# Performance work log

Measured on AMD Instinct MI355X. Metric: run time of the kernel, lower is better.

The kernel has to match this reference:

```python
import jax, jax.numpy as jnp
import numpy as np

IGNORE_INDEX = -100


def setup_inputs() -> dict:
    key = jax.random.key(0)
    k1, k2, k3 = jax.random.split(key, 3)
    N, H, V = 8192, 4096, 32000
    x = jax.random.normal(k1, (N, H), dtype=jnp.float32)
    # kaiming_uniform-like init scale for weight (V, H)
    bound = float(np.sqrt(6.0 / H))
    weight = jax.random.uniform(k2, (V, H), dtype=jnp.float32, minval=-bound, maxval=bound)
    target = jax.random.randint(k3, (N,), 0, V, dtype=jnp.int64)
    return {"x": x, "weight": weight, "target": target}


def reference(x, weight, target):
    # Fused linear (lm_head) + cross entropy, reduction='mean', ignore_index=-100.
    # logits: (N, V)
    logits = jnp.einsum('nh,vh->nv', x, weight)
    logp = jax.nn.log_softmax(logits, axis=-1)
    valid = target != IGNORE_INDEX
    safe_tgt = jnp.where(valid, target, 0)
    # NLL of the target class per token
    nll = -jnp.take_along_axis(logp, safe_tgt[:, None], axis=1)[:, 0]
    nll = jnp.where(valid, nll, 0.0)
    denom = jnp.maximum(valid.sum(), 1).astype(nll.dtype)
    return nll.sum() / denom
```

## Files before the change

### kernel.cpp

```cpp
#include <hip/hip_runtime.h>
#include <hip/hip_bf16.h>
#include <stdint.h>

typedef __attribute__((ext_vector_type(8))) __bf16 bf16x8;
typedef __attribute__((ext_vector_type(8))) unsigned short us8;
typedef __attribute__((ext_vector_type(4))) float f32x4;

#define BM 128
#define BN 128
#define BK 64

__device__ inline float bf2f(unsigned short u) {
  unsigned v = ((unsigned)u) << 16;
  float f;
  __builtin_memcpy(&f, &v, 4);
  return f;
}

__device__ inline unsigned short f2bf(float f) {
  unsigned u;
  __builtin_memcpy(&u, &f, 4);
  unsigned r = 0x7FFFu + ((u >> 16) & 1u);
  u += r;
  return (unsigned short)(u >> 16);
}

__device__ inline void gload16(const void* g, void* l) {
  __builtin_amdgcn_global_load_lds(
      (const __attribute__((address_space(1))) unsigned int*)g,
      (__attribute__((address_space(3))) unsigned int*)l, 16, 0, 0);
}

__global__ void cvt_kernel(const float* __restrict__ in,
                           unsigned short* __restrict__ out, int n4) {
  int i = blockIdx.x * blockDim.x + threadIdx.x;
  int stride = gridDim.x * blockDim.x;
  const float4* in4 = reinterpret_cast<const float4*>(in);
  ushort4* out4 = reinterpret_cast<ushort4*>(out);
  for (int idx = i; idx < n4; idx += stride) {
    float4 v = in4[idx];
    ushort4 o;
    o.x = f2bf(v.x); o.y = f2bf(v.y); o.z = f2bf(v.z); o.w = f2bf(v.w);
    out4[idx] = o;
  }
}

__launch_bounds__(256, 2)
__global__ void gemm_lse_kernel(const unsigned short* __restrict__ xb,
                                const unsigned short* __restrict__ wb,
                                float* __restrict__ pm, float* __restrict__ ps,
                                int N, int H, int V) {
  __shared__ __align__(16) unsigned short Als[BM * BK];
  __shared__ __align__(16) unsigned short Bls[BN * BK];

  const int tid = threadIdx.x;
  const int l = tid & 63;
  const int w = tid >> 6;
  const int wr = w >> 1, wc = w & 1;

  const int nwg = gridDim.x;
  const int chunk = nwg >> 3;
  const int id = blockIdx.x;
  const int sid = (id & 7) * chunk + (id >> 3);
  const int num_mb = N / BM;
  const int mb = sid % num_mb;
  const int vb = sid / num_mb;

  const int brow = mb * BM;
  const int bcol = vb * BN;

  f32x4 acc[4][4];
#pragma unroll
  for (int mi = 0; mi < 4; ++mi)
#pragma unroll
    for (int ni = 0; ni < 4; ++ni)
      acc[mi][ni] = (f32x4){0.f, 0.f, 0.f, 0.f};

  const int lrow = l >> 3;
  const int lcol = (l & 7) * 8;

  for (int kt = 0; kt < H; kt += BK) {
#pragma unroll
    for (int t = 0; t < 4; ++t) {
      const int c = w * 4 + t;
      const unsigned short* src =
          xb + (size_t)(brow + c * 8 + lrow) * H + kt + lcol;
      gload16(src, &Als[c * 512]);
    }
#pragma unroll
    for (int t = 0; t < 4; ++t) {
      const int c = w * 4 + t;
      const unsigned short* src =
          wb + (size_t)(bcol + c * 8 + lrow) * H + kt + lcol;
      gload16(src, &Bls[c * 512]);
    }
    __syncthreads();

#pragma unroll
    for (int ks = 0; ks < 2; ++ks) {
      bf16x8 af[4], bfr[4];
#pragma unroll
      for (int mi = 0; mi < 4; ++mi)
        af[mi] = *reinterpret_cast<const bf16x8*>(
            &Als[(wr * 64 + mi * 16 + (l & 15)) * BK + ks * 32 + (l >> 4) * 8]);
#pragma unroll
      for (int ni = 0; ni < 4; ++ni)
        bfr[ni] = *reinterpret_cast<const bf16x8*>(
            &Bls[(wc * 64 + ni * 16 + (l & 15)) * BK + ks * 32 + (l >> 4) * 8]);
#pragma unroll
      for (int mi = 0; mi < 4; ++mi)
#pragma unroll
        for (int ni = 0; ni < 4; ++ni)
          acc[mi][ni] = __builtin_amdgcn_mfma_f32_16x16x32_bf16(
              af[mi], bfr[ni], acc[mi][ni], 0, 0, 0);
    }
    __syncthreads();
  }

  float mrow[4][4], srow[4][4];
#pragma unroll
  for (int mi = 0; mi < 4; ++mi) {
#pragma unroll
    for (int j = 0; j < 4; ++j) {
      float m = acc[mi][0][j];
#pragma unroll
      for (int ni = 1; ni < 4; ++ni) m = fmaxf(m, acc[mi][ni][j]);
#pragma unroll
      for (int off = 1; off < 16; off <<= 1)
        m = fmaxf(m, __shfl_xor(m, off, 64));
      float s = 0.f;
#pragma unroll
      for (int ni = 0; ni < 4; ++ni) s += __expf(acc[mi][ni][j] - m);
#pragma unroll
      for (int off = 1; off < 16; off <<= 1) s += __shfl_xor(s, off, 64);
      mrow[mi][j] = m;
      srow[mi][j] = s;
    }
  }

  float* red_m = (float*)(void*)Als;
  float* red_s = red_m + 256;
  if ((l & 15) == 0) {
    const int g = l >> 4;
#pragma unroll
    for (int mi = 0; mi < 4; ++mi)
#pragma unroll
      for (int j = 0; j < 4; ++j) {
        const int row = wr * 64 + mi * 16 + g * 4 + j;
        red_m[wc * 128 + row] = mrow[mi][j];
        red_s[wc * 128 + row] = srow[mi][j];
      }
  }
  __syncthreads();
  if (tid < 128) {
    const int row = tid;
    const float m0 = red_m[row], m1 = red_m[128 + row];
    const float s0 = red_s[row], s1 = red_s[128 + row];
    const float M = fmaxf(m0, m1);
    const float S = s0 * __expf(m0 - M) + s1 * __expf(m1 - M);
    const size_t o = (size_t)vb * N + brow + row;
    pm[o] = M;
    ps[o] = S;
  }
}

__global__ void reduce_kernel(const float* __restrict__ pm,
                              const float* __restrict__ ps,
                              const unsigned short* __restrict__ xb,
                              const unsigned short* __restrict__ wb,
                              const int* __restrict__ tgt,
                              float* __restrict__ accum,
                              int N, int H, int nvb) {
  const int l = threadIdx.x & 63;
  const int w = threadIdx.x >> 6;
  const int row = blockIdx.x * 4 + w;
  if (row >= N) return;

  float M = -INFINITY, S = 0.f;
  for (int vb = l; vb < nvb; vb += 64) {
    const float m = pm[(size_t)vb * N + row];
    const float s = ps[(size_t)vb * N + row];
    const float nM = fmaxf(M, m);
    S = S * __expf(M - nM) + s * __expf(m - nM);
    M = nM;
  }
#pragma unroll
  for (int off = 1; off < 64; off <<= 1) {
    const float om = __shfl_xor(M, off, 64);
    const float os = __shfl_xor(S, off, 64);
    const float nM = fmaxf(M, om);
    S = S * __expf(M - nM) + os * __expf(om - nM);
    M = nM;
  }

  const int t = tgt[row];
  const bool valid = (t != -100);
  float dot = 0.f;
  if (valid) {
    const unsigned short* xr = xb + (size_t)row * H;
    const unsigned short* wrow = wb + (size_t)t * H;
    for (int k = l * 8; k < H; k += 64 * 8) {
      const us8 xv = *reinterpret_cast<const us8*>(xr + k);
      const us8 wv = *reinterpret_cast<const us8*>(wrow + k);
#pragma unroll
      for (int j = 0; j < 8; ++j) dot += bf2f(xv[j]) * bf2f(wv[j]);
    }
#pragma unroll
    for (int off = 1; off < 64; off <<= 1) dot += __shfl_xor(dot, off, 64);
  }

  if (l == 0) {
    const float lse = M + __logf(S);
    const float nll = valid ? (lse - dot) : 0.f;
    atomicAdd(&accum[0], nll);
    if (valid) atomicAdd(&accum[1], 1.f);
  }
}

__global__ void finalize_kernel(const float* __restrict__ accum,
                                float* __restrict__ out) {
  out[0] = accum[0] / fmaxf(accum[1], 1.f);
}

extern "C" void kernel_launch(void* const* d_in, const int* in_sizes, int n_in,
                              void* d_out, int out_size, void* d_ws,
                              size_t ws_size, hipStream_t stream) {
  const float* x = (const float*)d_in[0];
  const float* wt = (const float*)d_in[1];
  const int* tgt = (const int*)d_in[2];
  float* out = (float*)d_out;

  const int N = in_sizes[2];
  const int H = in_sizes[0] / N;
  const int V = in_sizes[1] / H;
  const int nvb = V / BN;
  const int nmb = N / BM;

  unsigned char* ws = (unsigned char*)d_ws;
  unsigned short* xb = (unsigned short*)ws;
  size_t off = (size_t)N * H * 2;
  unsigned short* wb = (unsigned short*)(ws + off);
  off += (size_t)V * H * 2;
  float* pm = (float*)(ws + off);
  off += (size_t)nvb * N * 4;
  float* ps = (float*)(ws + off);
  off += (size_t)nvb * N * 4;
  float* accum = (float*)(ws + off);

  hipMemsetAsync(accum, 0, 2 * sizeof(float), stream);

  cvt_kernel<<<2048, 256, 0, stream>>>(x, xb, (int)(((size_t)N * H) / 4));
  cvt_kernel<<<4096, 256, 0, stream>>>(wt, wb, (int)(((size_t)V * H) / 4));
  gemm_lse_kernel<<<nmb * nvb, 256, 0, stream>>>(xb, wb, pm, ps, N, H, V);
  reduce_kernel<<<N / 4, 256, 0, stream>>>(pm, ps, xb, wb, tgt, accum, N, H, nvb);
  finalize_kernel<<<1, 1, 0, stream>>>(accum, out);
}
```

Baseline: 3.614 ms.

## Use 256x256 double-buffered swizzled LDS tiles with 8-wave interleaved MFMA schedule

The GEMM+LSE kernel moves from 128x128 tiles with 4 waves and a single LDS buffer to 256x256 tiles with 8 waves. It double-buffers 128KB of LDS with an XOR-swizzled layout to avoid bank conflicts. Prefetches of the next K tile are split into halves and interleaved with four MFMA quadrant phases, using explicit barriers, waitcnts and setprio, so global loads overlap compute and each loaded tile is reused more. The tile count along K is hardcoded to 64, which assumes H=4096. The larger LDS footprint also limits occupancy to one block per CU.

```diff
diff --git a/kernel.cpp b/kernel.cpp
--- a/kernel.cpp
+++ b/kernel.cpp
@@ -6,9 +6,10 @@
 typedef __attribute__((ext_vector_type(8))) unsigned short us8;
 typedef __attribute__((ext_vector_type(4))) float f32x4;
 
-#define BM 128
-#define BN 128
+#define BM 256
+#define BN 256
 #define BK 64
+#define NT_TILES 64
 
 __device__ inline float bf2f(unsigned short u) {
   unsigned v = ((unsigned)u) << 16;
@@ -20,8 +21,7 @@
 __device__ inline unsigned short f2bf(float f) {
   unsigned u;
   __builtin_memcpy(&u, &f, 4);
-  unsigned r = 0x7FFFu + ((u >> 16) & 1u);
-  u += r;
+  u += 0x7FFFu + ((u >> 16) & 1u);
   return (unsigned short)(u >> 16);
 }
 
@@ -45,119 +45,191 @@
   }
 }
 
-__launch_bounds__(256, 2)
+__launch_bounds__(512, 2)
 __global__ void gemm_lse_kernel(const unsigned short* __restrict__ xb,
                                 const unsigned short* __restrict__ wb,
                                 float* __restrict__ pm, float* __restrict__ ps,
                                 int N, int H, int V) {
-  __shared__ __align__(16) unsigned short Als[BM * BK];
-  __shared__ __align__(16) unsigned short Bls[BN * BK];
+  __shared__ __align__(16) unsigned char lds[131072];
 
   const int tid = threadIdx.x;
   const int l = tid & 63;
   const int w = tid >> 6;
-  const int wr = w >> 1, wc = w & 1;
+  const int wm = w >> 2;
+  const int wn = w & 3;
 
   const int nwg = gridDim.x;
   const int chunk = nwg >> 3;
-  const int id = blockIdx.x;
-  const int sid = (id & 7) * chunk + (id >> 3);
-  const int num_mb = N / BM;
-  const int mb = sid % num_mb;
-  const int vb = sid / num_mb;
-
-  const int brow = mb * BM;
-  const int bcol = vb * BN;
-
-  f32x4 acc[4][4];
-#pragma unroll
-  for (int mi = 0; mi < 4; ++mi)
-#pragma unroll
-    for (int ni = 0; ni < 4; ++ni)
-      acc[mi][ni] = (f32x4){0.f, 0.f, 0.f, 0.f};
-
-  const int lrow = l >> 3;
-  const int lcol = (l & 7) * 8;
-
-  for (int kt = 0; kt < H; kt += BK) {
-#pragma unroll
-    for (int t = 0; t < 4; ++t) {
-      const int c = w * 4 + t;
-      const unsigned short* src =
-          xb + (size_t)(brow + c * 8 + lrow) * H + kt + lcol;
-      gload16(src, &Als[c * 512]);
-    }
-#pragma unroll
-    for (int t = 0; t < 4; ++t) {
-      const int c = w * 4 + t;
-      const unsigned short* src =
-          wb + (size_t)(bcol + c * 8 + lrow) * H + kt + lcol;
-      gload16(src, &Bls[c * 512]);
-    }
-    __syncthreads();
-
-#pragma unroll
-    for (int ks = 0; ks < 2; ++ks) {
-      bf16x8 af[4], bfr[4];
-#pragma unroll
-      for (int mi = 0; mi < 4; ++mi)
-        af[mi] = *reinterpret_cast<const bf16x8*>(
-            &Als[(wr * 64 + mi * 16 + (l & 15)) * BK + ks * 32 + (l >> 4) * 8]);
-#pragma unroll
-      for (int ni = 0; ni < 4; ++ni)
-        bfr[ni] = *reinterpret_cast<const bf16x8*>(
-            &Bls[(wc * 64 + ni * 16 + (l & 15)) * BK + ks * 32 + (l >> 4) * 8]);
-#pragma unroll
-      for (int mi = 0; mi < 4; ++mi)
-#pragma unroll
-        for (int ni = 0; ni < 4; ++ni)
-          acc[mi][ni] = __builtin_amdgcn_mfma_f32_16x16x32_bf16(
-              af[mi], bfr[ni], acc[mi][ni], 0, 0, 0);
-    }
-    __syncthreads();
-  }
-
-  float mrow[4][4], srow[4][4];
-#pragma unroll
-  for (int mi = 0; mi < 4; ++mi) {
+  const int sid = (blockIdx.x & 7) * chunk + (blockIdx.x >> 3);
+  const int nmb = N / BM;
+  const int mb = sid % nmb;
+  const int vb = sid / nmb;
+  const int brow = mb * BM, bcol = vb * BN;
+
+  const int r8 = tid >> 3;
+  const int c2src = ((tid & 7) << 4) ^ ((r8 & 7) << 4);
+  const unsigned short* srcA = xb + (size_t)(brow + r8) * H + (c2src >> 1);
+  const unsigned short* srcB = wb + (size_t)(bcol + r8) * H + (c2src >> 1);
+  const int wofs = (tid & 448) << 4;
+
+#define STAGE_A(buf, h, g, kt)                                          \
+  gload16(srcA + (size_t)((h) * 128 + (g) * 64) * H + (kt),             \
+          lds + (buf) * 65536 + (h) * 16384 + (g) * 8192 + wofs)
+#define STAGE_B(buf, h, g, kt)                                          \
+  gload16(srcB + (size_t)((h) * 128 + (g) * 64) * H + (kt),             \
+          lds + (buf) * 65536 + 32768 + (h) * 16384 + (g) * 8192 + wofs)
+
+  const int rA = (wm * 128 + (l & 15)) * 128;
+  const int rB = (wn * 64 + (l & 15)) * 128;
+  const int col0 = (((l >> 4) * 16)) ^ ((l & 7) << 4);
+  const int col1 = col0 ^ 64;
+
+  f32x4 acc[8][4];
+#pragma unroll
+  for (int mi = 0; mi < 8; ++mi)
+#pragma unroll
+    for (int ni = 0; ni < 4; ++ni) acc[mi][ni] = (f32x4){0.f, 0.f, 0.f, 0.f};
+
+  bf16x8 afr[4][2];
+  bf16x8 bfr[4][2];
+
+  STAGE_A(0, 0, 0, 0); STAGE_A(0, 0, 1, 0); STAGE_A(0, 1, 0, 0); STAGE_A(0, 1, 1, 0);
+  STAGE_B(0, 0, 0, 0); STAGE_B(0, 0, 1, 0); STAGE_B(0, 1, 0, 0); STAGE_B(0, 1, 1, 0);
+  asm volatile("s_waitcnt vmcnt(0)" ::: "memory");
+  __builtin_amdgcn_s_barrier();
+
+#pragma unroll 2
+  for (int t = 0; t < NT_TILES; ++t) {
+    const int cur = t & 1;
+    const int nxt = cur ^ 1;
+    const int ktn = (t + 1) * BK;
+    const bool pre = (t + 1 < NT_TILES);
+    char* pa = (char*)lds + cur * 65536;
+    char* pb = pa + 32768;
+
+#pragma unroll
+    for (int q = 0; q < 4; ++q) {
+      afr[q][0] = *(const bf16x8*)(pa + rA + q * 2048 + col0);
+      afr[q][1] = *(const bf16x8*)(pa + rA + q * 2048 + col1);
+    }
+#pragma unroll
+    for (int n = 0; n < 2; ++n) {
+      bfr[n][0] = *(const bf16x8*)(pb + rB + n * 2048 + col0);
+      bfr[n][1] = *(const bf16x8*)(pb + rB + n * 2048 + col1);
+    }
+    if (pre) {
+      STAGE_A(nxt, 0, 0, ktn); STAGE_A(nxt, 0, 1, ktn);
+      STAGE_B(nxt, 0, 0, ktn); STAGE_B(nxt, 0, 1, ktn);
+    }
+    __builtin_amdgcn_s_barrier();
+    asm volatile("s_waitcnt lgkmcnt(0)" ::: "memory");
+    __builtin_amdgcn_sched_barrier(0);
+    __builtin_amdgcn_s_setprio(1);
+#pragma unroll
+    for (int q = 0; q < 4; ++q)
+#pragma unroll
+      for (int n = 0; n < 2; ++n) {
+        acc[q][n] = __builtin_amdgcn_mfma_f32_16x16x32_bf16(afr[q][0], bfr[n][0], acc[q][n], 0, 0, 0);
+        acc[q][n] = __builtin_amdgcn_mfma_f32_16x16x32_bf16(afr[q][1], bfr[n][1], acc[q][n], 0, 0, 0);
+      }
+    __builtin_amdgcn_s_setprio(0);
+    __builtin_amdgcn_s_barrier();
+
+#pragma unroll
+    for (int n = 0; n < 2; ++n) {
+      bfr[2 + n][0] = *(const bf16x8*)(pb + rB + (2 + n) * 2048 + col0);
+      bfr[2 + n][1] = *(const bf16x8*)(pb + rB + (2 + n) * 2048 + col1);
+    }
+    if (pre) {
+      STAGE_A(nxt, 1, 0, ktn); STAGE_A(nxt, 1, 1, ktn);
+      STAGE_B(nxt, 1, 0, ktn); STAGE_B(nxt, 1, 1, ktn);
+    }
+    __builtin_amdgcn_s_barrier();
+    asm volatile("s_waitcnt lgkmcnt(0)" ::: "memory");
+    __builtin_amdgcn_sched_barrier(0);
+    __builtin_amdgcn_s_setprio(1);
+#pragma unroll
+    for (int q = 0; q < 4; ++q)
+#pragma unroll
+      for (int n = 0; n < 2; ++n) {
+        acc[q][2 + n] = __builtin_amdgcn_mfma_f32_16x16x32_bf16(afr[q][0], bfr[2 + n][0], acc[q][2 + n], 0, 0, 0);
+        acc[q][2 + n] = __builtin_amdgcn_mfma_f32_16x16x32_bf16(afr[q][1], bfr[2 + n][1], acc[q][2 + n], 0, 0, 0);
+      }
+    __builtin_amdgcn_s_setprio(0);
+    __builtin_amdgcn_s_barrier();
+
+#pragma unroll
+    for (int q = 0; q < 4; ++q) {
+      afr[q][0] = *(const bf16x8*)(pa + rA + (4 + q) * 2048 + col0);
+      afr[q][1] = *(const bf16x8*)(pa + rA + (4 + q) * 2048 + col1);
+    }
+    __builtin_amdgcn_s_barrier();
+    asm volatile("s_waitcnt lgkmcnt(0)" ::: "memory");
+    __builtin_amdgcn_sched_barrier(0);
+    __builtin_amdgcn_s_setprio(1);
+#pragma unroll
+    for (int q = 0; q < 4; ++q)
+#pragma unroll
+      for (int n = 0; n < 2; ++n) {
+        acc[4 + q][2 + n] = __builtin_amdgcn_mfma_f32_16x16x32_bf16(afr[q][0], bfr[2 + n][0], acc[4 + q][2 + n], 0, 0, 0);
+        acc[4 + q][2 + n] = __builtin_amdgcn_mfma_f32_16x16x32_bf16(afr[q][1], bfr[2 + n][1], acc[4 + q][2 + n], 0, 0, 0);
+      }
+    __builtin_amdgcn_s_setprio(0);
+    __builtin_amdgcn_s_barrier();
+
+    asm volatile("s_waitcnt vmcnt(0)" ::: "memory");
+    __builtin_amdgcn_s_barrier();
+    __builtin_amdgcn_sched_barrier(0);
+    __builtin_amdgcn_s_setprio(1);
+#pragma unroll
+    for (int q = 0; q < 4; ++q)
+#pragma unroll
+      for (int n = 0; n < 2; ++n) {
+        acc[4 + q][n] = __builtin_amdgcn_mfma_f32_16x16x32_bf16(afr[q][0], bfr[n][0], acc[4 + q][n], 0, 0, 0);
+        acc[4 + q][n] = __builtin_amdgcn_mfma_f32_16x16x32_bf16(afr[q][1], bfr[n][1], acc[4 + q][n], 0, 0, 0);
+      }
+    __builtin_amdgcn_s_setprio(0);
+    __builtin_amdgcn_s_barrier();
+  }
+#undef STAGE_A
+#undef STAGE_B
+
+  __syncthreads();
+  float* redm = (float*)(void*)lds;
+  float* reds = (float*)(void*)(lds + 4096);
+
+#pragma unroll
+  for (int mi = 0; mi < 8; ++mi) {
 #pragma unroll
     for (int j = 0; j < 4; ++j) {
       float m = acc[mi][0][j];
 #pragma unroll
-      for (int ni = 1; ni < 4; ++ni) m = fmaxf(m, acc[mi][ni][j]);
-#pragma unroll
-      for (int off = 1; off < 16; off <<= 1)
-        m = fmaxf(m, __shfl_xor(m, off, 64));
+      for (int n = 1; n < 4; ++n) m = fmaxf(m, acc[mi][n][j]);
+#pragma unroll
+      for (int off = 1; off < 16; off <<= 1) m = fmaxf(m, __shfl_xor(m, off, 64));
       float s = 0.f;
 #pragma unroll
-      for (int ni = 0; ni < 4; ++ni) s += __expf(acc[mi][ni][j] - m);
+      for (int n = 0; n < 4; ++n) s += __expf(acc[mi][n][j] - m);
 #pragma unroll
       for (int off = 1; off < 16; off <<= 1) s += __shfl_xor(s, off, 64);
-      mrow[mi][j] = m;
-      srow[mi][j] = s;
-    }
-  }
-
-  float* red_m = (float*)(void*)Als;
-  float* red_s = red_m + 256;
-  if ((l & 15) == 0) {
-    const int g = l >> 4;
-#pragma unroll
-    for (int mi = 0; mi < 4; ++mi)
-#pragma unroll
-      for (int j = 0; j < 4; ++j) {
-        const int row = wr * 64 + mi * 16 + g * 4 + j;
-        red_m[wc * 128 + row] = mrow[mi][j];
-        red_s[wc * 128 + row] = srow[mi][j];
-      }
+      if ((l & 15) == 0) {
+        const int row = wm * 128 + mi * 16 + (l >> 4) * 4 + j;
+        redm[wn * 256 + row] = m;
+        reds[wn * 256 + row] = s;
+      }
+    }
   }
   __syncthreads();
-  if (tid < 128) {
+  if (tid < 256) {
     const int row = tid;
-    const float m0 = red_m[row], m1 = red_m[128 + row];
-    const float s0 = red_s[row], s1 = red_s[128 + row];
-    const float M = fmaxf(m0, m1);
-    const float S = s0 * __expf(m0 - M) + s1 * __expf(m1 - M);
+    float M = redm[row];
+    M = fmaxf(M, redm[256 + row]);
+    M = fmaxf(M, redm[512 + row]);
+    M = fmaxf(M, redm[768 + row]);
+    float S = 0.f;
+#pragma unroll
+    for (int k = 0; k < 4; ++k)
+      S += reds[k * 256 + row] * __expf(redm[k * 256 + row] - M);
     const size_t o = (size_t)vb * N + brow + row;
     pm[o] = M;
     ps[o] = S;
@@ -251,7 +323,7 @@
 
   cvt_kernel<<<2048, 256, 0, stream>>>(x, xb, (int)(((size_t)N * H) / 4));
   cvt_kernel<<<4096, 256, 0, stream>>>(wt, wb, (int)(((size_t)V * H) / 4));
-  gemm_lse_kernel<<<nmb * nvb, 256, 0, stream>>>(xb, wb, pm, ps, N, H, V);
+  gemm_lse_kernel<<<nmb * nvb, 512, 0, stream>>>(xb, wb, pm, ps, N, H, V);
   reduce_kernel<<<N / 4, 256, 0, stream>>>(pm, ps, xb, wb, tgt, accum, N, H, nvb);
   finalize_kernel<<<1, 1, 0, stream>>>(accum, out);
 }
```

After: 3.149 ms. -12.9%, faster.
